# Kernel tuning notes

Hardware: AMD Instinct MI355X
Metric: run time of the kernel (lower is better)

Reference implementation:

```python
import jax, jax.numpy as jnp
import numpy as np

B, C, L = 4, 256, 4096
NUM_GROUPS = 32
EPS = 1e-6


def setup_inputs() -> dict:
    key = jax.random.key(0)
    ks = jax.random.split(key, 8)
    s = 1.0 / np.sqrt(C)  # conv1x1 init scale
    return {
        "x": jax.random.normal(ks[0], (B, C, L), dtype=jnp.float32),
        "norm_g": jnp.ones((C,), dtype=jnp.float32),
        "norm_b": jnp.zeros((C,), dtype=jnp.float32),
        "q_w": jax.random.normal(ks[1], (C, C), dtype=jnp.float32) * s,
        "q_b": jnp.zeros((C,), dtype=jnp.float32),
        "k_w": jax.random.normal(ks[2], (C, C), dtype=jnp.float32) * s,
        "k_b": jnp.zeros((C,), dtype=jnp.float32),
        "v_w": jax.random.normal(ks[3], (C, C), dtype=jnp.float32) * s,
        "v_b": jnp.zeros((C,), dtype=jnp.float32),
        "proj_w": jax.random.normal(ks[4], (C, C), dtype=jnp.float32) * s,
        "proj_b": jnp.zeros((C,), dtype=jnp.float32),
    }


def _group_norm(x, g, b):
    # x: [B, C, L] -> groups of C//NUM_GROUPS channels
    Bx, Cx, Lx = x.shape
    xg = x.reshape(Bx, NUM_GROUPS, Cx // NUM_GROUPS, Lx)
    mean = jnp.mean(xg, axis=(2, 3), keepdims=True)
    var = jnp.var(xg, axis=(2, 3), keepdims=True)
    xn = ((xg - mean) * jax.lax.rsqrt(var + EPS)).reshape(Bx, Cx, Lx)
    return xn * g[None, :, None] + b[None, :, None]


def _conv1x1(w, b, h):
    # w: [Cout, Cin], h: [B, Cin, L]
    return jnp.einsum("oc,bcl->bol", w, h) + b[None, :, None]


def reference(x, norm_g, norm_b, q_w, q_b, k_w, k_b, v_w, v_b, proj_w, proj_b):
    h = _group_norm(x, norm_g, norm_b)
    q = _conv1x1(q_w, q_b, h)   # [B, C, L]
    k = _conv1x1(k_w, k_b, h)
    v = _conv1x1(v_w, v_b, h)

    scale = jnp.asarray(x.shape[1], x.dtype) ** -0.5
    # w_[b,i,j] = sum_c q[b,c,i] * k[b,c,j]
    w_ = jnp.einsum("bci,bcj->bij", q, k) * scale
    w_ = jax.nn.softmax(w_, axis=2)
    # h_[b,c,i] = sum_j v[b,c,j] * w_[b,i,j]
    h2 = jnp.einsum("bcj,bij->bci", v, w_)

    out = _conv1x1(proj_w, proj_b, h2)
    return x + out
```

## Files before the change

kernel.cpp:

```cpp
#include <hip/hip_runtime.h>

#define B_ 4
#define C_ 256
#define L_ 4096
#define NG 32
#define CPG 8
#define BL (B_ * L_)
#define KPART 4
#define KEYS_PP (L_ / KPART)
#define QLOG2E 0.09016844f

typedef __attribute__((ext_vector_type(8))) __bf16 bf16x8;
typedef __attribute__((ext_vector_type(8))) short s16x8;
typedef __attribute__((ext_vector_type(4))) float f32x4;
typedef __attribute__((ext_vector_type(16))) float f32x16;

__device__ __forceinline__ unsigned short f2bf(float f) {
  unsigned int u = __builtin_bit_cast(unsigned int, f);
  u += 0x7fffu + ((u >> 16) & 1u);
  return (unsigned short)(u >> 16);
}
__device__ __forceinline__ float bf2f(unsigned short u) {
  unsigned int v = ((unsigned int)u) << 16;
  return __builtin_bit_cast(float, v);
}
#if __has_builtin(__builtin_amdgcn_exp2f)
#define EXP2F(x) __builtin_amdgcn_exp2f(x)
#else
#define EXP2F(x) exp2f(x)
#endif

__device__ __forceinline__ void gld_lds16(const void* g, void* l) {
  __builtin_amdgcn_global_load_lds(
      (const __attribute__((address_space(1))) unsigned int*)g,
      (__attribute__((address_space(3))) unsigned int*)l, 16, 0, 0);
}

__device__ __forceinline__ float red16_add(float x) {
  int i;
  i = __builtin_amdgcn_update_dpp(0, __builtin_bit_cast(int, x), 0xB1, 0xF, 0xF, false);
  x += __builtin_bit_cast(float, i);
  i = __builtin_amdgcn_update_dpp(0, __builtin_bit_cast(int, x), 0x4E, 0xF, 0xF, false);
  x += __builtin_bit_cast(float, i);
  i = __builtin_amdgcn_update_dpp(0, __builtin_bit_cast(int, x), 0x124, 0xF, 0xF, false);
  x += __builtin_bit_cast(float, i);
  i = __builtin_amdgcn_update_dpp(0, __builtin_bit_cast(int, x), 0x128, 0xF, 0xF, false);
  x += __builtin_bit_cast(float, i);
  return x;
}

__global__ __launch_bounds__(256) void init_k(const float* __restrict__ qw,
                                              const float* __restrict__ kw,
                                              const float* __restrict__ vw,
                                              const float* __restrict__ pw,
                                              const float* __restrict__ qb,
                                              const float* __restrict__ x,
                                              unsigned short* __restrict__ wq,
                                              unsigned short* __restrict__ wk,
                                              unsigned short* __restrict__ wv,
                                              unsigned short* __restrict__ wp,
                                              float* __restrict__ qbs,
                                              float* __restrict__ stats) {
  const int bid = blockIdx.x;
  const int t = threadIdx.x;
  if (bid < 128) {
    const int m = bid >> 5;
    const int blk = bid & 31;
    const float* src = (m == 0) ? qw : (m == 1) ? kw : (m == 2) ? vw : pw;
    unsigned short* dst = (m == 0) ? wq : (m == 1) ? wk : (m == 2) ? wv : wp;
    const float sc = (m == 0) ? QLOG2E : 1.0f;
    const int base = (blk * 256 + t) * 8;
    f32x4 a = *(const f32x4*)(src + base);
    f32x4 b = *(const f32x4*)(src + base + 4);
    s16x8 o;
#pragma unroll
    for (int j = 0; j < 4; ++j) {
      o[j] = (short)f2bf(a[j] * sc);
      o[4 + j] = (short)f2bf(b[j] * sc);
    }
    *(s16x8*)(dst + base) = o;
    if (m == 0 && blk == 0) qbs[t] = qb[t] * QLOG2E;
  } else {
    const int bg = bid - 128;
    const float* base = x + (size_t)bg * (CPG * L_);
    float s = 0.f, ss = 0.f;
#pragma unroll
    for (int i = 0; i < 32; ++i) {
      f32x4 v = *(const f32x4*)(base + (size_t)(t + i * 256) * 4);
#pragma unroll
      for (int j = 0; j < 4; ++j) { s += v[j]; ss += v[j] * v[j]; }
    }
#pragma unroll
    for (int d = 1; d < 64; d <<= 1) {
      s += __shfl_xor(s, d, 64);
      ss += __shfl_xor(ss, d, 64);
    }
    __shared__ float red[8];
    if ((t & 63) == 0) { red[(t >> 6) * 2] = s; red[(t >> 6) * 2 + 1] = ss; }
    __syncthreads();
    if (t == 0) {
      float S = red[0] + red[2] + red[4] + red[6];
      float SS = red[1] + red[3] + red[5] + red[7];
      const float inv_n = 1.f / (float)(CPG * L_);
      float mean = S * inv_n;
      float var = SS * inv_n - mean * mean;
      stats[bg * 2] = mean;
      stats[bg * 2 + 1] = rsqrtf(var + 1e-6f);
    }
  }
}

__global__ __launch_bounds__(256) void gn_apply_k(const float* __restrict__ x,
                                                  const float* __restrict__ stats,
                                                  const float* __restrict__ gam,
                                                  const float* __restrict__ bet,
                                                  unsigned short* __restrict__ ht) {
  __shared__ unsigned short tile[64 * 256];
  const int blk = blockIdx.x;
  const int b = blk >> 6;
  const int l0 = (blk & 63) * 64;
  const int t = threadIdx.x;
  const int c = t;
  const float mean = stats[(b * NG + (c >> 3)) * 2];
  const float rstd = stats[(b * NG + (c >> 3)) * 2 + 1];
  const float sc = rstd * gam[c];
  const float sb = bet[c] - mean * sc;
  const float* row = x + ((size_t)(b * C_ + c)) * L_ + l0;
#pragma unroll
  for (int v = 0; v < 16; ++v) {
    f32x4 f = *(const f32x4*)(row + v * 4);
#pragma unroll
    for (int j = 0; j < 4; ++j) tile[(v * 4 + j) * 256 + c] = f2bf(f[j] * sc + sb);
  }
  __syncthreads();
#pragma unroll
  for (int i = 0; i < 8; ++i) {
    int id = t + i * 256;
    int l = id >> 5, off = id & 31;
    *(s16x8*)(ht + ((size_t)(b * L_) + l0 + l) * 256 + off * 8) =
        *(const s16x8*)(tile + l * 256 + off * 8);
  }
}

__global__ __launch_bounds__(256) void qkv_k(const unsigned short* __restrict__ ht,
                                             const unsigned short* __restrict__ wq,
                                             const unsigned short* __restrict__ wk,
                                             const unsigned short* __restrict__ wv,
                                             const float* __restrict__ qbs,
                                             const float* __restrict__ kbias,
                                             const float* __restrict__ vbias,
                                             unsigned short* __restrict__ qt,
                                             unsigned short* __restrict__ kt,
                                             unsigned short* __restrict__ vg) {
  __shared__ unsigned short Al[64 * 256];
  __shared__ unsigned short Wl[64 * 256];
  const int z = blockIdx.z;
  const unsigned short* W = (z == 0) ? wq : (z == 1) ? wk : wv;
  const float* bias = (z == 0) ? qbs : (z == 1) ? kbias : vbias;
  const int m0 = blockIdx.x * 64;
  const int n0 = blockIdx.y * 64;
  const int t = threadIdx.x;
  const int w = t >> 6, lane = t & 63, l15 = lane & 15, q = lane >> 4;
#pragma unroll
  for (int i = 0; i < 8; ++i) {
    const int seg = w * 8 + i;
    const int idx = seg * 64 + lane;
    const int row = idx >> 5, c16 = idx & 31;
    gld_lds16(ht + (size_t)(m0 + row) * 256 + ((c16 ^ (row & 7)) * 8), Al + seg * 512);
    gld_lds16(W + (size_t)(n0 + row) * 256 + ((c16 ^ (row & 7)) * 8), Wl + seg * 512);
  }
  __syncthreads();
  bf16x8 af[8];
#pragma unroll
  for (int kf = 0; kf < 8; ++kf) {
    int row = w * 16 + l15;
    af[kf] = *(const bf16x8*)(Al + row * 256 + (((kf * 4 + q) ^ (row & 7)) * 8));
  }
  f32x4 acc[4];
#pragma unroll
  for (int nf = 0; nf < 4; ++nf) {
    f32x4 cacc = {0.f, 0.f, 0.f, 0.f};
#pragma unroll
    for (int kf = 0; kf < 8; ++kf) {
      int row = nf * 16 + l15;
      bf16x8 bf = *(const bf16x8*)(Wl + row * 256 + (((kf * 4 + q) ^ (row & 7)) * 8));
      cacc = __builtin_amdgcn_mfma_f32_16x16x32_bf16(af[kf], bf, cacc, 0, 0, 0);
    }
    acc[nf] = cacc;
  }
  unsigned short* Ct = (z == 0) ? qt : kt;
#pragma unroll
  for (int nf = 0; nf < 4; ++nf) {
    const int n = n0 + nf * 16 + l15;
    const float bs = bias[n];
#pragma unroll
    for (int r = 0; r < 4; ++r) {
      const int m = m0 + w * 16 + q * 4 + r;
      const float v = acc[nf][r] + bs;
      if (z < 2) {
        Ct[(size_t)m * 256 + n] = f2bf(v);
      } else {
        const int b = m >> 12, i = m & (L_ - 1);
        const int jt = i >> 5, jj = i & 31;
        const int qc = jj >> 3, pos = jj & 7;
        vg[((size_t)(b * 128 + jt)) * 8192 + n * 32 + ((qc ^ ((n >> 1) & 3)) * 8) + pos] =
            f2bf(v);
      }
    }
  }
}

__global__ __launch_bounds__(256) void proj_k(const unsigned short* __restrict__ X,
                                              const unsigned short* __restrict__ W,
                                              const float* __restrict__ bias,
                                              const float* __restrict__ xres,
                                              float* __restrict__ out) {
  __shared__ unsigned short Wl[64 * 256];
  __shared__ unsigned short Xl[64 * 256];
  const int i0 = blockIdx.x * 64;
  const int o0 = blockIdx.y * 64;
  const int b = blockIdx.z;
  const int t = threadIdx.x;
  const int w = t >> 6, lane = t & 63, l15 = lane & 15, q = lane >> 4;
#pragma unroll
  for (int i = 0; i < 8; ++i) {
    const int seg = w * 8 + i;
    const int idx = seg * 64 + lane;
    const int row = idx >> 5, c16 = idx & 31;
    gld_lds16(W + (size_t)(o0 + row) * 256 + ((c16 ^ (row & 7)) * 8), Wl + seg * 512);
    gld_lds16(X + ((size_t)(b * L_) + i0 + row) * 256 + ((c16 ^ (row & 7)) * 8),
              Xl + seg * 512);
  }
  __syncthreads();
  bf16x8 af[8];
#pragma unroll
  for (int kf = 0; kf < 8; ++kf) {
    int row = w * 16 + l15;
    af[kf] = *(const bf16x8*)(Wl + row * 256 + (((kf * 4 + q) ^ (row & 7)) * 8));
  }
  f32x4 acc[4];
#pragma unroll
  for (int nf = 0; nf < 4; ++nf) {
    f32x4 cacc = {0.f, 0.f, 0.f, 0.f};
#pragma unroll
    for (int kf = 0; kf < 8; ++kf) {
      int row = nf * 16 + l15;
      bf16x8 bf = *(const bf16x8*)(Xl + row * 256 + (((kf * 4 + q) ^ (row & 7)) * 8));
      cacc = __builtin_amdgcn_mfma_f32_16x16x32_bf16(af[kf], bf, cacc, 0, 0, 0);
    }
    acc[nf] = cacc;
  }
#pragma unroll
  for (int nf = 0; nf < 4; ++nf) {
    const int i = i0 + nf * 16 + l15;
#pragma unroll
    for (int r = 0; r < 4; ++r) {
      const int o = o0 + w * 16 + q * 4 + r;
      const size_t idx = ((size_t)(b * C_ + o)) * L_ + i;
      out[idx] = acc[nf][r] + bias[o] + xres[idx];
    }
  }
}

__global__ __launch_bounds__(256, 2) void attn_k(const unsigned short* __restrict__ Qt,
                                                 const unsigned short* __restrict__ Kt,
                                                 const unsigned short* __restrict__ Vg,
                                                 unsigned short* __restrict__ op01,
                                                 unsigned short* __restrict__ op23,
                                                 float* __restrict__ ml) {
  __shared__ unsigned short Kl[32 * 256];
  __shared__ unsigned short Vl[256 * 32];
  __shared__ unsigned short Pl[4 * 32 * 40];
  const int bid = blockIdx.x;
  const int g = bid & 15;
  const int b = g >> 2, part = g & 3;
  const int qi = bid >> 4;
  const int t = threadIdx.x;
  const int w = t >> 6, lane = t & 63;
  const int l15 = lane & 15, q = lane >> 4;
  const int l31 = lane & 31, h = lane >> 5;

  const int qrow0 = b * L_ + qi * 128 + w * 32;
  bf16x8 qf[2][8];
#pragma unroll
  for (int mi = 0; mi < 2; ++mi)
#pragma unroll
    for (int kf = 0; kf < 8; ++kf)
      qf[mi][kf] =
          *(const bf16x8*)(Qt + ((size_t)(qrow0 + mi * 16 + l15)) * 256 + kf * 32 + q * 8);

  f32x16 oacc[8];
#pragma unroll
  for (int nf = 0; nf < 8; ++nf)
#pragma unroll
    for (int gg = 0; gg < 16; ++gg) oacc[nf][gg] = 0.f;
  float ls0[4] = {0.f, 0.f, 0.f, 0.f}, ls1[4] = {0.f, 0.f, 0.f, 0.f};

  const unsigned short* kbase = Kt + ((size_t)(b * L_ + part * KEYS_PP)) * 256;
  const unsigned short* vbase = Vg + ((size_t)(b * 128 + part * 32)) * 8192;
  unsigned short* Pw = Pl + w * 1280;

  for (int it = 0; it < KEYS_PP / 32; ++it) {
    __syncthreads();
    {
      const unsigned short* ksrc = kbase + (size_t)(it * 32) * 256;
      const unsigned short* vsrc = vbase + (size_t)it * 8192;
#pragma unroll
      for (int i = 0; i < 4; ++i) {
        const int seg = w * 4 + i;
        const int idx = seg * 64 + lane;
        const int row = idx >> 5, c16 = idx & 31;
        gld_lds16(ksrc + (size_t)row * 256 + ((c16 ^ (row & 7)) * 8), Kl + seg * 512);
        gld_lds16(vsrc + (size_t)idx * 8, Vl + seg * 512);
      }
    }
    __syncthreads();

    f32x4 s00 = {0.f, 0.f, 0.f, 0.f}, s01 = s00, s10 = s00, s11 = s00;
#pragma unroll
    for (int kf = 0; kf < 8; ++kf) {
      const int ch = ((kf * 4 + q) ^ (l15 & 7)) * 8;
      bf16x8 kb0 = *(const bf16x8*)(Kl + l15 * 256 + ch);
      bf16x8 kb1 = *(const bf16x8*)(Kl + (16 + l15) * 256 + ch);
      s00 = __builtin_amdgcn_mfma_f32_16x16x32_bf16(qf[0][kf], kb0, s00, 0, 0, 0);
      s01 = __builtin_amdgcn_mfma_f32_16x16x32_bf16(qf[0][kf], kb1, s01, 0, 0, 0);
      s10 = __builtin_amdgcn_mfma_f32_16x16x32_bf16(qf[1][kf], kb0, s10, 0, 0, 0);
      s11 = __builtin_amdgcn_mfma_f32_16x16x32_bf16(qf[1][kf], kb1, s11, 0, 0, 0);
    }
#pragma unroll
    for (int r = 0; r < 4; ++r) {
      float p00 = EXP2F(s00[r]), p01 = EXP2F(s01[r]);
      float p10 = EXP2F(s10[r]), p11 = EXP2F(s11[r]);
      ls0[r] += p00 + p01;
      ls1[r] += p10 + p11;
      Pw[(q * 4 + r) * 40 + l15] = f2bf(p00);
      Pw[(q * 4 + r) * 40 + 16 + l15] = f2bf(p01);
      Pw[(16 + q * 4 + r) * 40 + l15] = f2bf(p10);
      Pw[(16 + q * 4 + r) * 40 + 16 + l15] = f2bf(p11);
    }
    __syncthreads();

    bf16x8 va[2][2];
#pragma unroll
    for (int nf = 0; nf < 2; ++nf) {
      const int c = w * 64 + nf * 32 + l31;
#pragma unroll
      for (int kc = 0; kc < 2; ++kc)
        va[nf][kc] =
            *(const bf16x8*)(Vl + c * 32 + (((kc * 2 + h) ^ ((c >> 1) & 3)) * 8));
    }
#pragma unroll
    for (int qt2 = 0; qt2 < 4; ++qt2) {
      bf16x8 pa0 = *(const bf16x8*)(Pl + qt2 * 1280 + l31 * 40 + h * 8);
      bf16x8 pa1 = *(const bf16x8*)(Pl + qt2 * 1280 + l31 * 40 + 16 + h * 8);
#pragma unroll
      for (int nf = 0; nf < 2; ++nf) {
        oacc[qt2 * 2 + nf] =
            __builtin_amdgcn_mfma_f32_32x32x16_bf16(pa0, va[nf][0], oacc[qt2 * 2 + nf], 0, 0, 0);
        oacc[qt2 * 2 + nf] =
            __builtin_amdgcn_mfma_f32_32x32x16_bf16(pa1, va[nf][1], oacc[qt2 * 2 + nf], 0, 0, 0);
      }
    }
  }

  unsigned short* opb = (part < 2) ? op01 + (size_t)part * BL * 256
                                   : op23 + (size_t)(part - 2) * BL * 256;
  const int qb0 = b * L_ + qi * 128;
#pragma unroll
  for (int qt2 = 0; qt2 < 4; ++qt2)
#pragma unroll
    for (int nf = 0; nf < 2; ++nf)
#pragma unroll
      for (int gg = 0; gg < 16; ++gg) {
        const int row = qt2 * 32 + (gg & 3) + 8 * (gg >> 2) + 4 * h;
        opb[(size_t)(qb0 + row) * 256 + w * 64 + nf * 32 + l31] =
            f2bf(oacc[qt2 * 2 + nf][gg]);
      }
#pragma unroll
  for (int r = 0; r < 4; ++r) {
    ls0[r] = red16_add(ls0[r]);
    ls1[r] = red16_add(ls1[r]);
  }
  if (l15 == 0) {
    float* mlp = ml + (size_t)part * BL;
#pragma unroll
    for (int r = 0; r < 4; ++r) {
      mlp[qrow0 + q * 4 + r] = ls0[r];
      mlp[qrow0 + 16 + q * 4 + r] = ls1[r];
    }
  }
}

__global__ __launch_bounds__(256) void merge_k(const unsigned short* __restrict__ op01,
                                               const unsigned short* __restrict__ op23,
                                               const float* __restrict__ ml,
                                               unsigned short* __restrict__ Om) {
  const int row = blockIdx.x * 8 + (threadIdx.x >> 5);
  const int c8 = threadIdx.x & 31;
  const float inv = 1.0f / (ml[row] + ml[BL + row] + ml[2 * BL + row] + ml[3 * BL + row]);
  const size_t off = (size_t)row * 256 + c8 * 8;
  s16x8 v0 = *(const s16x8*)(op01 + off);
  s16x8 v1 = *(const s16x8*)(op01 + (size_t)BL * 256 + off);
  s16x8 v2 = *(const s16x8*)(op23 + off);
  s16x8 v3 = *(const s16x8*)(op23 + (size_t)BL * 256 + off);
  s16x8 o;
#pragma unroll
  for (int j = 0; j < 8; ++j)
    o[j] = (short)f2bf((bf2f((unsigned short)v0[j]) + bf2f((unsigned short)v1[j]) +
                        bf2f((unsigned short)v2[j]) + bf2f((unsigned short)v3[j])) *
                       inv);
  *(s16x8*)(Om + off) = o;
}

extern "C" void kernel_launch(void* const* d_in, const int* in_sizes, int n_in,
                              void* d_out, int out_size, void* d_ws, size_t ws_size,
                              hipStream_t stream) {
  const float* x = (const float*)d_in[0];
  const float* norm_g = (const float*)d_in[1];
  const float* norm_b = (const float*)d_in[2];
  const float* q_w = (const float*)d_in[3];
  const float* q_b = (const float*)d_in[4];
  const float* k_w = (const float*)d_in[5];
  const float* k_b = (const float*)d_in[6];
  const float* v_w = (const float*)d_in[7];
  const float* v_b = (const float*)d_in[8];
  const float* p_w = (const float*)d_in[9];
  const float* p_b = (const float*)d_in[10];
  float* out = (float*)d_out;
  (void)in_sizes; (void)n_in; (void)out_size; (void)ws_size;

  char* ws = (char*)d_ws;
  const size_t MB = 1u << 20;
  float* stats = (float*)ws;
  float* qbs = (float*)(ws + 1024);
  unsigned short* wq = (unsigned short*)(ws + 4096);
  unsigned short* wk = wq + 65536;
  unsigned short* wv = wk + 65536;
  unsigned short* wp = wv + 65536;
  unsigned short* ht = (unsigned short*)(ws + 1 * MB);
  unsigned short* qt = (unsigned short*)(ws + 9 * MB);
  unsigned short* kt = (unsigned short*)(ws + 17 * MB);
  unsigned short* vg = (unsigned short*)(ws + 25 * MB);
  unsigned short* op23 = (unsigned short*)(ws + 33 * MB);
  float* ml = (float*)(ws + 50 * MB);
  unsigned short* op01 = (unsigned short*)d_out;

  init_k<<<256, 256, 0, stream>>>(q_w, k_w, v_w, p_w, q_b, x, wq, wk, wv, wp, qbs, stats);
  gn_apply_k<<<B_ * (L_ / 64), 256, 0, stream>>>(x, stats, norm_g, norm_b, ht);
  qkv_k<<<dim3((B_ * L_) / 64, C_ / 64, 3), 256, 0, stream>>>(ht, wq, wk, wv, qbs, k_b,
                                                              v_b, qt, kt, vg);
  attn_k<<<512, 256, 0, stream>>>(qt, kt, vg, op01, op23, ml);
  merge_k<<<BL / 8, 256, 0, stream>>>(op01, op23, ml, ht);
  proj_k<<<dim3(L_ / 64, C_ / 64, B_), 256, 0, stream>>>(ht, wp, p_b, x, out);
}
```

Before: 223.4 us.

## Fuse split-K merge into projection and pipeline V loads in attention

The attention kernel stops staging V through shared memory. Each wave reads V directly from global memory into registers in a new interleaved layout, and the P tile is double-buffered so the PV MFMAs for step it-1 run after the K prefetch for step it+1 is issued. When the workspace is large enough, the separate merge kernel is removed. The projection kernel instead accumulates over all four partial outputs and applies the softmax normaliser per row in its epilogue. This saves a kernel launch and one round trip of the merged tensor, but projection now does four times the MFMA work and LDS loads, and uncached V global reads may add latency.

```diff
diff --git a/kernel.cpp b/kernel.cpp
--- a/kernel.cpp
+++ b/kernel.cpp
@@ -8,6 +8,7 @@
 #define BL (B_ * L_)
 #define KPART 4
 #define KEYS_PP (L_ / KPART)
+#define NIT (KEYS_PP / 32)
 #define QLOG2E 0.09016844f
 
 typedef __attribute__((ext_vector_type(8))) __bf16 bf16x8;
@@ -201,19 +202,201 @@
         Ct[(size_t)m * 256 + n] = f2bf(v);
       } else {
         const int b = m >> 12, i = m & (L_ - 1);
-        const int jt = i >> 5, jj = i & 31;
-        const int qc = jj >> 3, pos = jj & 7;
-        vg[((size_t)(b * 128 + jt)) * 8192 + n * 32 + ((qc ^ ((n >> 1) & 3)) * 8) + pos] =
-            f2bf(v);
-      }
-    }
-  }
-}
-
+        const int jt = i >> 5, j = i & 31;
+        const int slot = (j & 15) * 2 + (j >> 4);
+        vg[((size_t)(b * 128 + jt)) * 8192 + n * 32 + slot] = f2bf(v);
+      }
+    }
+  }
+}
+
+__global__ __launch_bounds__(256, 2) void attn_k(const unsigned short* __restrict__ Qt,
+                                                 const unsigned short* __restrict__ Kt,
+                                                 const unsigned short* __restrict__ Vg,
+                                                 unsigned short* __restrict__ o0p,
+                                                 unsigned short* __restrict__ o1p,
+                                                 unsigned short* __restrict__ o2p,
+                                                 unsigned short* __restrict__ o3p,
+                                                 float* __restrict__ ml) {
+  __shared__ unsigned short Kl[32 * 256];
+  __shared__ unsigned int Pb[2][4][32][20];
+  const int bid = blockIdx.x;
+  const int g = bid & 15;
+  const int b = g >> 2, part = g & 3;
+  const int qi = bid >> 4;
+  const int t = threadIdx.x;
+  const int w = t >> 6, lane = t & 63;
+  const int l15 = lane & 15, q = lane >> 4;
+  const int l31 = lane & 31, h = lane >> 5;
+
+  const int qb0 = b * L_ + qi * 128;
+  const int qrow0 = qb0 + w * 32;
+  bf16x8 qf[2][8];
+#pragma unroll
+  for (int mi = 0; mi < 2; ++mi)
+#pragma unroll
+    for (int kf = 0; kf < 8; ++kf)
+      qf[mi][kf] =
+          *(const bf16x8*)(Qt + ((size_t)(qrow0 + mi * 16 + l15)) * 256 + kf * 32 + q * 8);
+
+  f32x16 oacc[8];
+#pragma unroll
+  for (int nf = 0; nf < 8; ++nf)
+#pragma unroll
+    for (int gg = 0; gg < 16; ++gg) oacc[nf][gg] = 0.f;
+  float ls0[4] = {0.f, 0.f, 0.f, 0.f}, ls1[4] = {0.f, 0.f, 0.f, 0.f};
+
+  const unsigned short* kbase = Kt + ((size_t)(b * L_ + part * KEYS_PP)) * 256;
+  const unsigned short* vbase = Vg + ((size_t)(b * 128 + part * 32)) * 8192;
+
+#pragma unroll
+  for (int i = 0; i < 4; ++i) {
+    const int seg = w * 4 + i;
+    const int idx = seg * 64 + lane;
+    const int row = idx >> 5, c16 = idx & 31;
+    gld_lds16(kbase + (size_t)row * 256 + ((c16 ^ (row & 7)) * 8), Kl + seg * 512);
+  }
+
+  for (int it = 0; it < NIT; ++it) {
+    __syncthreads();
+    bf16x8 va[2][2];
+    if (it > 0) {
+      const unsigned short* vt = vbase + (size_t)(it - 1) * 8192;
+#pragma unroll
+      for (int nf = 0; nf < 2; ++nf)
+#pragma unroll
+        for (int kc = 0; kc < 2; ++kc)
+          va[nf][kc] = *(const bf16x8*)(vt + (w * 64 + nf * 32 + l31) * 32 +
+                                        kc * 16 + h * 8);
+    }
+    f32x4 s00 = {0.f, 0.f, 0.f, 0.f}, s01 = s00, s10 = s00, s11 = s00;
+#pragma unroll
+    for (int kf = 0; kf < 8; ++kf) {
+      const int ch = ((kf * 4 + q) ^ (l15 & 7)) * 8;
+      bf16x8 kb0 = *(const bf16x8*)(Kl + l15 * 256 + ch);
+      bf16x8 kb1 = *(const bf16x8*)(Kl + (16 + l15) * 256 + ch);
+      s00 = __builtin_amdgcn_mfma_f32_16x16x32_bf16(qf[0][kf], kb0, s00, 0, 0, 0);
+      s01 = __builtin_amdgcn_mfma_f32_16x16x32_bf16(qf[0][kf], kb1, s01, 0, 0, 0);
+      s10 = __builtin_amdgcn_mfma_f32_16x16x32_bf16(qf[1][kf], kb0, s10, 0, 0, 0);
+      s11 = __builtin_amdgcn_mfma_f32_16x16x32_bf16(qf[1][kf], kb1, s11, 0, 0, 0);
+    }
+    const int buf = it & 1;
+#pragma unroll
+    for (int r = 0; r < 4; ++r) {
+      float p00 = EXP2F(s00[r]), p01 = EXP2F(s01[r]);
+      float p10 = EXP2F(s10[r]), p11 = EXP2F(s11[r]);
+      ls0[r] += p00 + p01;
+      ls1[r] += p10 + p11;
+      Pb[buf][w][q * 4 + r][l15] = (unsigned int)f2bf(p00) | ((unsigned int)f2bf(p01) << 16);
+      Pb[buf][w][16 + q * 4 + r][l15] =
+          (unsigned int)f2bf(p10) | ((unsigned int)f2bf(p11) << 16);
+    }
+    __syncthreads();
+    if (it + 1 < NIT) {
+      const unsigned short* ksrc = kbase + (size_t)((it + 1) * 32) * 256;
+#pragma unroll
+      for (int i = 0; i < 4; ++i) {
+        const int seg = w * 4 + i;
+        const int idx = seg * 64 + lane;
+        const int row = idx >> 5, c16 = idx & 31;
+        gld_lds16(ksrc + (size_t)row * 256 + ((c16 ^ (row & 7)) * 8), Kl + seg * 512);
+      }
+    }
+    if (it > 0) {
+      const int pbuf = (it - 1) & 1;
+#pragma unroll
+      for (int qt2 = 0; qt2 < 4; ++qt2) {
+        bf16x8 pa0 = *(const bf16x8*)&Pb[pbuf][qt2][l31][h * 4];
+        bf16x8 pa1 = *(const bf16x8*)&Pb[pbuf][qt2][l31][8 + h * 4];
+#pragma unroll
+        for (int nf = 0; nf < 2; ++nf) {
+          oacc[qt2 * 2 + nf] =
+              __builtin_amdgcn_mfma_f32_32x32x16_bf16(pa0, va[nf][0], oacc[qt2 * 2 + nf], 0, 0, 0);
+          oacc[qt2 * 2 + nf] =
+              __builtin_amdgcn_mfma_f32_32x32x16_bf16(pa1, va[nf][1], oacc[qt2 * 2 + nf], 0, 0, 0);
+        }
+      }
+    }
+  }
+  {
+    bf16x8 va[2][2];
+    const unsigned short* vt = vbase + (size_t)(NIT - 1) * 8192;
+#pragma unroll
+    for (int nf = 0; nf < 2; ++nf)
+#pragma unroll
+      for (int kc = 0; kc < 2; ++kc)
+        va[nf][kc] =
+            *(const bf16x8*)(vt + (w * 64 + nf * 32 + l31) * 32 + kc * 16 + h * 8);
+    const int pbuf = (NIT - 1) & 1;
+#pragma unroll
+    for (int qt2 = 0; qt2 < 4; ++qt2) {
+      bf16x8 pa0 = *(const bf16x8*)&Pb[pbuf][qt2][l31][h * 4];
+      bf16x8 pa1 = *(const bf16x8*)&Pb[pbuf][qt2][l31][8 + h * 4];
+#pragma unroll
+      for (int nf = 0; nf < 2; ++nf) {
+        oacc[qt2 * 2 + nf] =
+            __builtin_amdgcn_mfma_f32_32x32x16_bf16(pa0, va[nf][0], oacc[qt2 * 2 + nf], 0, 0, 0);
+        oacc[qt2 * 2 + nf] =
+            __builtin_amdgcn_mfma_f32_32x32x16_bf16(pa1, va[nf][1], oacc[qt2 * 2 + nf], 0, 0, 0);
+      }
+    }
+  }
+
+  unsigned short* opb = (part == 0) ? o0p : (part == 1) ? o1p : (part == 2) ? o2p : o3p;
+#pragma unroll
+  for (int qt2 = 0; qt2 < 4; ++qt2)
+#pragma unroll
+    for (int nf = 0; nf < 2; ++nf)
+#pragma unroll
+      for (int gg = 0; gg < 16; ++gg) {
+        const int row = qt2 * 32 + (gg & 3) + 8 * (gg >> 2) + 4 * h;
+        opb[(size_t)(qb0 + row) * 256 + w * 64 + nf * 32 + l31] =
+            f2bf(oacc[qt2 * 2 + nf][gg]);
+      }
+#pragma unroll
+  for (int r = 0; r < 4; ++r) {
+    ls0[r] = red16_add(ls0[r]);
+    ls1[r] = red16_add(ls1[r]);
+  }
+  if (l15 == 0) {
+    float* mlp = ml + (size_t)part * BL;
+#pragma unroll
+    for (int r = 0; r < 4; ++r) {
+      mlp[qrow0 + q * 4 + r] = ls0[r];
+      mlp[qrow0 + 16 + q * 4 + r] = ls1[r];
+    }
+  }
+}
+
+__global__ __launch_bounds__(256) void merge_k(const unsigned short* __restrict__ o0p,
+                                               const unsigned short* __restrict__ o1p,
+                                               const unsigned short* __restrict__ o2p,
+                                               const unsigned short* __restrict__ o3p,
+                                               const float* __restrict__ ml,
+                                               unsigned short* __restrict__ Om) {
+  const int row = blockIdx.x * 8 + (threadIdx.x >> 5);
+  const int c8 = threadIdx.x & 31;
+  const float inv = 1.0f / (ml[row] + ml[BL + row] + ml[2 * BL + row] + ml[3 * BL + row]);
+  const size_t off = (size_t)row * 256 + c8 * 8;
+  s16x8 v0 = *(const s16x8*)(o0p + off);
+  s16x8 v1 = *(const s16x8*)(o1p + off);
+  s16x8 v2 = *(const s16x8*)(o2p + off);
+  s16x8 v3 = *(const s16x8*)(o3p + off);
+  s16x8 o;
+#pragma unroll
+  for (int j = 0; j < 8; ++j)
+    o[j] = (short)f2bf((bf2f((unsigned short)v0[j]) + bf2f((unsigned short)v1[j]) +
+                        bf2f((unsigned short)v2[j]) + bf2f((unsigned short)v3[j])) *
+                       inv);
+  *(s16x8*)(Om + off) = o;
+}
+
+template <int FUSED>
 __global__ __launch_bounds__(256) void proj_k(const unsigned short* __restrict__ X,
                                               const unsigned short* __restrict__ W,
                                               const float* __restrict__ bias,
                                               const float* __restrict__ xres,
+                                              const float* __restrict__ ml,
                                               float* __restrict__ out) {
   __shared__ unsigned short Wl[64 * 256];
   __shared__ unsigned short Xl[64 * 256];
@@ -222,6 +405,7 @@
   const int b = blockIdx.z;
   const int t = threadIdx.x;
   const int w = t >> 6, lane = t & 63, l15 = lane & 15, q = lane >> 4;
+  const int NP = FUSED ? 4 : 1;
 #pragma unroll
   for (int i = 0; i < 8; ++i) {
     const int seg = w * 8 + i;
@@ -238,178 +422,48 @@
     int row = w * 16 + l15;
     af[kf] = *(const bf16x8*)(Wl + row * 256 + (((kf * 4 + q) ^ (row & 7)) * 8));
   }
-  f32x4 acc[4];
-#pragma unroll
-  for (int nf = 0; nf < 4; ++nf) {
-    f32x4 cacc = {0.f, 0.f, 0.f, 0.f};
-#pragma unroll
-    for (int kf = 0; kf < 8; ++kf) {
-      int row = nf * 16 + l15;
-      bf16x8 bf = *(const bf16x8*)(Xl + row * 256 + (((kf * 4 + q) ^ (row & 7)) * 8));
-      cacc = __builtin_amdgcn_mfma_f32_16x16x32_bf16(af[kf], bf, cacc, 0, 0, 0);
-    }
-    acc[nf] = cacc;
+  f32x4 acc[4] = {{0.f, 0.f, 0.f, 0.f}, {0.f, 0.f, 0.f, 0.f},
+                  {0.f, 0.f, 0.f, 0.f}, {0.f, 0.f, 0.f, 0.f}};
+  for (int p = 0; p < NP; ++p) {
+    if (p > 0) {
+      __syncthreads();
+#pragma unroll
+      for (int i = 0; i < 8; ++i) {
+        const int seg = w * 8 + i;
+        const int idx = seg * 64 + lane;
+        const int row = idx >> 5, c16 = idx & 31;
+        gld_lds16(X + ((size_t)p * BL + (size_t)(b * L_) + i0 + row) * 256 +
+                      ((c16 ^ (row & 7)) * 8),
+                  Xl + seg * 512);
+      }
+      __syncthreads();
+    }
+#pragma unroll
+    for (int nf = 0; nf < 4; ++nf) {
+      f32x4 cacc = acc[nf];
+#pragma unroll
+      for (int kf = 0; kf < 8; ++kf) {
+        int row = nf * 16 + l15;
+        bf16x8 bf = *(const bf16x8*)(Xl + row * 256 + (((kf * 4 + q) ^ (row & 7)) * 8));
+        cacc = __builtin_amdgcn_mfma_f32_16x16x32_bf16(af[kf], bf, cacc, 0, 0, 0);
+      }
+      acc[nf] = cacc;
+    }
   }
 #pragma unroll
   for (int nf = 0; nf < 4; ++nf) {
     const int i = i0 + nf * 16 + l15;
+    const int grow = b * L_ + i;
+    float sc = 1.0f;
+    if (FUSED)
+      sc = 1.0f / (ml[grow] + ml[BL + grow] + ml[2 * BL + grow] + ml[3 * BL + grow]);
 #pragma unroll
     for (int r = 0; r < 4; ++r) {
       const int o = o0 + w * 16 + q * 4 + r;
       const size_t idx = ((size_t)(b * C_ + o)) * L_ + i;
-      out[idx] = acc[nf][r] + bias[o] + xres[idx];
-    }
-  }
-}
-
-__global__ __launch_bounds__(256, 2) void attn_k(const unsigned short* __restrict__ Qt,
-                                                 const unsigned short* __restrict__ Kt,
-                                                 const unsigned short* __restrict__ Vg,
-                                                 unsigned short* __restrict__ op01,
-                                                 unsigned short* __restrict__ op23,
-                                                 float* __restrict__ ml) {
-  __shared__ unsigned short Kl[32 * 256];
-  __shared__ unsigned short Vl[256 * 32];
-  __shared__ unsigned short Pl[4 * 32 * 40];
-  const int bid = blockIdx.x;
-  const int g = bid & 15;
-  const int b = g >> 2, part = g & 3;
-  const int qi = bid >> 4;
-  const int t = threadIdx.x;
-  const int w = t >> 6, lane = t & 63;
-  const int l15 = lane & 15, q = lane >> 4;
-  const int l31 = lane & 31, h = lane >> 5;
-
-  const int qrow0 = b * L_ + qi * 128 + w * 32;
-  bf16x8 qf[2][8];
-#pragma unroll
-  for (int mi = 0; mi < 2; ++mi)
-#pragma unroll
-    for (int kf = 0; kf < 8; ++kf)
-      qf[mi][kf] =
-          *(const bf16x8*)(Qt + ((size_t)(qrow0 + mi * 16 + l15)) * 256 + kf * 32 + q * 8);
-
-  f32x16 oacc[8];
-#pragma unroll
-  for (int nf = 0; nf < 8; ++nf)
-#pragma unroll
-    for (int gg = 0; gg < 16; ++gg) oacc[nf][gg] = 0.f;
-  float ls0[4] = {0.f, 0.f, 0.f, 0.f}, ls1[4] = {0.f, 0.f, 0.f, 0.f};
-
-  const unsigned short* kbase = Kt + ((size_t)(b * L_ + part * KEYS_PP)) * 256;
-  const unsigned short* vbase = Vg + ((size_t)(b * 128 + part * 32)) * 8192;
-  unsigned short* Pw = Pl + w * 1280;
-
-  for (int it = 0; it < KEYS_PP / 32; ++it) {
-    __syncthreads();
-    {
-      const unsigned short* ksrc = kbase + (size_t)(it * 32) * 256;
-      const unsigned short* vsrc = vbase + (size_t)it * 8192;
-#pragma unroll
-      for (int i = 0; i < 4; ++i) {
-        const int seg = w * 4 + i;
-        const int idx = seg * 64 + lane;
-        const int row = idx >> 5, c16 = idx & 31;
-        gld_lds16(ksrc + (size_t)row * 256 + ((c16 ^ (row & 7)) * 8), Kl + seg * 512);
-        gld_lds16(vsrc + (size_t)idx * 8, Vl + seg * 512);
-      }
-    }
-    __syncthreads();
-
-    f32x4 s00 = {0.f, 0.f, 0.f, 0.f}, s01 = s00, s10 = s00, s11 = s00;
-#pragma unroll
-    for (int kf = 0; kf < 8; ++kf) {
-      const int ch = ((kf * 4 + q) ^ (l15 & 7)) * 8;
-      bf16x8 kb0 = *(const bf16x8*)(Kl + l15 * 256 + ch);
-      bf16x8 kb1 = *(const bf16x8*)(Kl + (16 + l15) * 256 + ch);
-      s00 = __builtin_amdgcn_mfma_f32_16x16x32_bf16(qf[0][kf], kb0, s00, 0, 0, 0);
-      s01 = __builtin_amdgcn_mfma_f32_16x16x32_bf16(qf[0][kf], kb1, s01, 0, 0, 0);
-      s10 = __builtin_amdgcn_mfma_f32_16x16x32_bf16(qf[1][kf], kb0, s10, 0, 0, 0);
-      s11 = __builtin_amdgcn_mfma_f32_16x16x32_bf16(qf[1][kf], kb1, s11, 0, 0, 0);
-    }
-#pragma unroll
-    for (int r = 0; r < 4; ++r) {
-      float p00 = EXP2F(s00[r]), p01 = EXP2F(s01[r]);
-      float p10 = EXP2F(s10[r]), p11 = EXP2F(s11[r]);
-      ls0[r] += p00 + p01;
-      ls1[r] += p10 + p11;
-      Pw[(q * 4 + r) * 40 + l15] = f2bf(p00);
-      Pw[(q * 4 + r) * 40 + 16 + l15] = f2bf(p01);
-      Pw[(16 + q * 4 + r) * 40 + l15] = f2bf(p10);
-      Pw[(16 + q * 4 + r) * 40 + 16 + l15] = f2bf(p11);
-    }
-    __syncthreads();
-
-    bf16x8 va[2][2];
-#pragma unroll
-    for (int nf = 0; nf < 2; ++nf) {
-      const int c = w * 64 + nf * 32 + l31;
-#pragma unroll
-      for (int kc = 0; kc < 2; ++kc)
-        va[nf][kc] =
-            *(const bf16x8*)(Vl + c * 32 + (((kc * 2 + h) ^ ((c >> 1) & 3)) * 8));
-    }
-#pragma unroll
-    for (int qt2 = 0; qt2 < 4; ++qt2) {
-      bf16x8 pa0 = *(const bf16x8*)(Pl + qt2 * 1280 + l31 * 40 + h * 8);
-      bf16x8 pa1 = *(const bf16x8*)(Pl + qt2 * 1280 + l31 * 40 + 16 + h * 8);
-#pragma unroll
-      for (int nf = 0; nf < 2; ++nf) {
-        oacc[qt2 * 2 + nf] =
-            __builtin_amdgcn_mfma_f32_32x32x16_bf16(pa0, va[nf][0], oacc[qt2 * 2 + nf], 0, 0, 0);
-        oacc[qt2 * 2 + nf] =
-            __builtin_amdgcn_mfma_f32_32x32x16_bf16(pa1, va[nf][1], oacc[qt2 * 2 + nf], 0, 0, 0);
-      }
-    }
-  }
-
-  unsigned short* opb = (part < 2) ? op01 + (size_t)part * BL * 256
-                                   : op23 + (size_t)(part - 2) * BL * 256;
-  const int qb0 = b * L_ + qi * 128;
-#pragma unroll
-  for (int qt2 = 0; qt2 < 4; ++qt2)
-#pragma unroll
-    for (int nf = 0; nf < 2; ++nf)
-#pragma unroll
-      for (int gg = 0; gg < 16; ++gg) {
-        const int row = qt2 * 32 + (gg & 3) + 8 * (gg >> 2) + 4 * h;
-        opb[(size_t)(qb0 + row) * 256 + w * 64 + nf * 32 + l31] =
-            f2bf(oacc[qt2 * 2 + nf][gg]);
-      }
-#pragma unroll
-  for (int r = 0; r < 4; ++r) {
-    ls0[r] = red16_add(ls0[r]);
-    ls1[r] = red16_add(ls1[r]);
-  }
-  if (l15 == 0) {
-    float* mlp = ml + (size_t)part * BL;
-#pragma unroll
-    for (int r = 0; r < 4; ++r) {
-      mlp[qrow0 + q * 4 + r] = ls0[r];
-      mlp[qrow0 + 16 + q * 4 + r] = ls1[r];
-    }
-  }
-}
-
-__global__ __launch_bounds__(256) void merge_k(const unsigned short* __restrict__ op01,
-                                               const unsigned short* __restrict__ op23,
-                                               const float* __restrict__ ml,
-                                               unsigned short* __restrict__ Om) {
-  const int row = blockIdx.x * 8 + (threadIdx.x >> 5);
-  const int c8 = threadIdx.x & 31;
-  const float inv = 1.0f / (ml[row] + ml[BL + row] + ml[2 * BL + row] + ml[3 * BL + row]);
-  const size_t off = (size_t)row * 256 + c8 * 8;
-  s16x8 v0 = *(const s16x8*)(op01 + off);
-  s16x8 v1 = *(const s16x8*)(op01 + (size_t)BL * 256 + off);
-  s16x8 v2 = *(const s16x8*)(op23 + off);
-  s16x8 v3 = *(const s16x8*)(op23 + (size_t)BL * 256 + off);
-  s16x8 o;
-#pragma unroll
-  for (int j = 0; j < 8; ++j)
-    o[j] = (short)f2bf((bf2f((unsigned short)v0[j]) + bf2f((unsigned short)v1[j]) +
-                        bf2f((unsigned short)v2[j]) + bf2f((unsigned short)v3[j])) *
-                       inv);
-  *(s16x8*)(Om + off) = o;
+      out[idx] = acc[nf][r] * sc + bias[o] + xres[idx];
+    }
+  }
 }
 
 extern "C" void kernel_launch(void* const* d_in, const int* in_sizes, int n_in,
@@ -427,29 +481,48 @@
   const float* p_w = (const float*)d_in[9];
   const float* p_b = (const float*)d_in[10];
   float* out = (float*)d_out;
-  (void)in_sizes; (void)n_in; (void)out_size; (void)ws_size;
+  (void)in_sizes; (void)n_in; (void)out_size;
 
   char* ws = (char*)d_ws;
   const size_t MB = 1u << 20;
+  const size_t PSZ = (size_t)BL * 256 * 2;
   float* stats = (float*)ws;
   float* qbs = (float*)(ws + 1024);
   unsigned short* wq = (unsigned short*)(ws + 4096);
   unsigned short* wk = wq + 65536;
   unsigned short* wv = wk + 65536;
   unsigned short* wp = wv + 65536;
+  float* ml = (float*)(ws + 640 * 1024);
   unsigned short* ht = (unsigned short*)(ws + 1 * MB);
   unsigned short* qt = (unsigned short*)(ws + 9 * MB);
   unsigned short* kt = (unsigned short*)(ws + 17 * MB);
   unsigned short* vg = (unsigned short*)(ws + 25 * MB);
-  unsigned short* op23 = (unsigned short*)(ws + 33 * MB);
-  float* ml = (float*)(ws + 50 * MB);
-  unsigned short* op01 = (unsigned short*)d_out;
+
+  const int fused = (ws_size >= 33 * MB + 4 * PSZ) ? 1 : 0;
+
+  unsigned short *o0p, *o1p, *o2p, *o3p;
+  if (fused) {
+    unsigned short* opcat = (unsigned short*)(ws + 33 * MB);
+    o0p = opcat;
+    o1p = opcat + PSZ / 2;
+    o2p = opcat + PSZ;
+    o3p = opcat + 3 * PSZ / 2;
+  } else {
+    o0p = (unsigned short*)d_out;
+    o1p = (unsigned short*)d_out + PSZ / 2;
+    o2p = (unsigned short*)(ws + 33 * MB);
+    o3p = o2p + PSZ / 2;
+  }
 
   init_k<<<256, 256, 0, stream>>>(q_w, k_w, v_w, p_w, q_b, x, wq, wk, wv, wp, qbs, stats);
   gn_apply_k<<<B_ * (L_ / 64), 256, 0, stream>>>(x, stats, norm_g, norm_b, ht);
   qkv_k<<<dim3((B_ * L_) / 64, C_ / 64, 3), 256, 0, stream>>>(ht, wq, wk, wv, qbs, k_b,
                                                               v_b, qt, kt, vg);
-  attn_k<<<512, 256, 0, stream>>>(qt, kt, vg, op01, op23, ml);
-  merge_k<<<BL / 8, 256, 0, stream>>>(op01, op23, ml, ht);
-  proj_k<<<dim3(L_ / 64, C_ / 64, B_), 256, 0, stream>>>(ht, wp, p_b, x, out);
-}
+  attn_k<<<512, 256, 0, stream>>>(qt, kt, vg, o0p, o1p, o2p, o3p, ml);
+  if (fused) {
+    proj_k<1><<<dim3(L_ / 64, C_ / 64, B_), 256, 0, stream>>>(o0p, wp, p_b, x, ml, out);
+  } else {
+    merge_k<<<BL / 8, 256, 0, stream>>>(o0p, o1p, o2p, o3p, ml, ht);
+    proj_k<0><<<dim3(L_ / 64, C_ / 64, B_), 256, 0, stream>>>(ht, wp, p_b, x, ml, out);
+  }
+}
```

New measurement: 237.9 us. 1.07x slower.

## Double-buffer K/V tiles and make each wave own its query rows in PV

Applied to the files above, without the earlier changes.

The attention kernel now double-buffers the K and V shared-memory tiles, prefetching the next key block while the current one is computed. This removes one of the two barriers per iteration. The PV step is restructured so each wave multiplies only its own 32 query rows against all 256 channels, which removes the barrier before reading other waves' P tiles. The cost is twice the LDS for K/V, which may lower occupancy below the requested 2 blocks/CU, and more V reads from LDS per wave. The partial-output buffer pointers and the ml location are also reorganized.

```diff
diff --git a/kernel.cpp b/kernel.cpp
--- a/kernel.cpp
+++ b/kernel.cpp
@@ -8,6 +8,7 @@
 #define BL (B_ * L_)
 #define KPART 4
 #define KEYS_PP (L_ / KPART)
+#define NIT (KEYS_PP / 32)
 #define QLOG2E 0.09016844f
 
 typedef __attribute__((ext_vector_type(8))) __bf16 bf16x8;
@@ -210,6 +211,155 @@
   }
 }
 
+__global__ __launch_bounds__(256, 2) void attn_k(const unsigned short* __restrict__ Qt,
+                                                 const unsigned short* __restrict__ Kt,
+                                                 const unsigned short* __restrict__ Vg,
+                                                 unsigned short* __restrict__ o0p,
+                                                 unsigned short* __restrict__ o1p,
+                                                 unsigned short* __restrict__ o2p,
+                                                 unsigned short* __restrict__ o3p,
+                                                 float* __restrict__ ml) {
+  __shared__ unsigned short Kl[2][32 * 256];
+  __shared__ unsigned short Vl[2][256 * 32];
+  __shared__ unsigned short Pl[4 * 32 * 40];
+  const int bid = blockIdx.x;
+  const int g = bid & 15;
+  const int b = g >> 2, part = g & 3;
+  const int qi = bid >> 4;
+  const int t = threadIdx.x;
+  const int w = t >> 6, lane = t & 63;
+  const int l15 = lane & 15, q = lane >> 4;
+  const int l31 = lane & 31, h = lane >> 5;
+
+  const int qb0 = b * L_ + qi * 128;
+  const int qrow0 = qb0 + w * 32;
+  bf16x8 qf[2][8];
+#pragma unroll
+  for (int mi = 0; mi < 2; ++mi)
+#pragma unroll
+    for (int kf = 0; kf < 8; ++kf)
+      qf[mi][kf] =
+          *(const bf16x8*)(Qt + ((size_t)(qrow0 + mi * 16 + l15)) * 256 + kf * 32 + q * 8);
+
+  f32x16 oacc[8];
+#pragma unroll
+  for (int nf = 0; nf < 8; ++nf)
+#pragma unroll
+    for (int gg = 0; gg < 16; ++gg) oacc[nf][gg] = 0.f;
+  float ls0[4] = {0.f, 0.f, 0.f, 0.f}, ls1[4] = {0.f, 0.f, 0.f, 0.f};
+
+  const unsigned short* kbase = Kt + ((size_t)(b * L_ + part * KEYS_PP)) * 256;
+  const unsigned short* vbase = Vg + ((size_t)(b * 128 + part * 32)) * 8192;
+  unsigned short* Pw = Pl + w * 1280;
+
+#pragma unroll
+  for (int i = 0; i < 4; ++i) {
+    const int seg = w * 4 + i;
+    const int idx = seg * 64 + lane;
+    const int row = idx >> 5, c16 = idx & 31;
+    gld_lds16(kbase + (size_t)row * 256 + ((c16 ^ (row & 7)) * 8), &Kl[0][0] + seg * 512);
+    gld_lds16(vbase + (size_t)idx * 8, &Vl[0][0] + seg * 512);
+  }
+
+  for (int it = 0; it < NIT; ++it) {
+    __syncthreads();
+    if (it + 1 < NIT) {
+      const unsigned short* ksrc = kbase + (size_t)((it + 1) * 32) * 256;
+      const unsigned short* vsrc = vbase + (size_t)(it + 1) * 8192;
+      unsigned short* kd = &Kl[(it + 1) & 1][0];
+      unsigned short* vd = &Vl[(it + 1) & 1][0];
+#pragma unroll
+      for (int i = 0; i < 4; ++i) {
+        const int seg = w * 4 + i;
+        const int idx = seg * 64 + lane;
+        const int row = idx >> 5, c16 = idx & 31;
+        gld_lds16(ksrc + (size_t)row * 256 + ((c16 ^ (row & 7)) * 8), kd + seg * 512);
+        gld_lds16(vsrc + (size_t)idx * 8, vd + seg * 512);
+      }
+    }
+    const unsigned short* Kb = &Kl[it & 1][0];
+    const unsigned short* Vb = &Vl[it & 1][0];
+
+    f32x4 s00 = {0.f, 0.f, 0.f, 0.f}, s01 = s00, s10 = s00, s11 = s00;
+#pragma unroll
+    for (int kf = 0; kf < 8; ++kf) {
+      const int ch = ((kf * 4 + q) ^ (l15 & 7)) * 8;
+      bf16x8 kb0 = *(const bf16x8*)(Kb + l15 * 256 + ch);
+      bf16x8 kb1 = *(const bf16x8*)(Kb + (16 + l15) * 256 + ch);
+      s00 = __builtin_amdgcn_mfma_f32_16x16x32_bf16(qf[0][kf], kb0, s00, 0, 0, 0);
+      s01 = __builtin_amdgcn_mfma_f32_16x16x32_bf16(qf[0][kf], kb1, s01, 0, 0, 0);
+      s10 = __builtin_amdgcn_mfma_f32_16x16x32_bf16(qf[1][kf], kb0, s10, 0, 0, 0);
+      s11 = __builtin_amdgcn_mfma_f32_16x16x32_bf16(qf[1][kf], kb1, s11, 0, 0, 0);
+    }
+#pragma unroll
+    for (int r = 0; r < 4; ++r) {
+      float p00 = EXP2F(s00[r]), p01 = EXP2F(s01[r]);
+      float p10 = EXP2F(s10[r]), p11 = EXP2F(s11[r]);
+      ls0[r] += p00 + p01;
+      ls1[r] += p10 + p11;
+      Pw[(q * 4 + r) * 40 + l15] = f2bf(p00);
+      Pw[(q * 4 + r) * 40 + 16 + l15] = f2bf(p01);
+      Pw[(16 + q * 4 + r) * 40 + l15] = f2bf(p10);
+      Pw[(16 + q * 4 + r) * 40 + 16 + l15] = f2bf(p11);
+    }
+    bf16x8 pa0 = *(const bf16x8*)(Pw + l31 * 40 + h * 8);
+    bf16x8 pa1 = *(const bf16x8*)(Pw + l31 * 40 + 16 + h * 8);
+#pragma unroll
+    for (int nf = 0; nf < 8; ++nf) {
+      const int c = nf * 32 + l31;
+      bf16x8 v0 = *(const bf16x8*)(Vb + c * 32 + ((h ^ ((c >> 1) & 3)) * 8));
+      bf16x8 v1 = *(const bf16x8*)(Vb + c * 32 + (((2 + h) ^ ((c >> 1) & 3)) * 8));
+      oacc[nf] = __builtin_amdgcn_mfma_f32_32x32x16_bf16(pa0, v0, oacc[nf], 0, 0, 0);
+      oacc[nf] = __builtin_amdgcn_mfma_f32_32x32x16_bf16(pa1, v1, oacc[nf], 0, 0, 0);
+    }
+  }
+
+  unsigned short* opb = (part == 0) ? o0p : (part == 1) ? o1p : (part == 2) ? o2p : o3p;
+#pragma unroll
+  for (int nf = 0; nf < 8; ++nf)
+#pragma unroll
+    for (int gg = 0; gg < 16; ++gg) {
+      const int row = (gg & 3) + 8 * (gg >> 2) + 4 * h;
+      opb[(size_t)(qrow0 + row) * 256 + nf * 32 + l31] = f2bf(oacc[nf][gg]);
+    }
+#pragma unroll
+  for (int r = 0; r < 4; ++r) {
+    ls0[r] = red16_add(ls0[r]);
+    ls1[r] = red16_add(ls1[r]);
+  }
+  if (l15 == 0) {
+    float* mlp = ml + (size_t)part * BL;
+#pragma unroll
+    for (int r = 0; r < 4; ++r) {
+      mlp[qrow0 + q * 4 + r] = ls0[r];
+      mlp[qrow0 + 16 + q * 4 + r] = ls1[r];
+    }
+  }
+}
+
+__global__ __launch_bounds__(256) void merge_k(const unsigned short* __restrict__ o0p,
+                                               const unsigned short* __restrict__ o1p,
+                                               const unsigned short* __restrict__ o2p,
+                                               const unsigned short* __restrict__ o3p,
+                                               const float* __restrict__ ml,
+                                               unsigned short* __restrict__ Om) {
+  const int row = blockIdx.x * 8 + (threadIdx.x >> 5);
+  const int c8 = threadIdx.x & 31;
+  const float inv = 1.0f / (ml[row] + ml[BL + row] + ml[2 * BL + row] + ml[3 * BL + row]);
+  const size_t off = (size_t)row * 256 + c8 * 8;
+  s16x8 v0 = *(const s16x8*)(o0p + off);
+  s16x8 v1 = *(const s16x8*)(o1p + off);
+  s16x8 v2 = *(const s16x8*)(o2p + off);
+  s16x8 v3 = *(const s16x8*)(o3p + off);
+  s16x8 o;
+#pragma unroll
+  for (int j = 0; j < 8; ++j)
+    o[j] = (short)f2bf((bf2f((unsigned short)v0[j]) + bf2f((unsigned short)v1[j]) +
+                        bf2f((unsigned short)v2[j]) + bf2f((unsigned short)v3[j])) *
+                       inv);
+  *(s16x8*)(Om + off) = o;
+}
+
 __global__ __launch_bounds__(256) void proj_k(const unsigned short* __restrict__ X,
                                               const unsigned short* __restrict__ W,
                                               const float* __restrict__ bias,
@@ -260,156 +410,6 @@
       out[idx] = acc[nf][r] + bias[o] + xres[idx];
     }
   }
-}
-
-__global__ __launch_bounds__(256, 2) void attn_k(const unsigned short* __restrict__ Qt,
-                                                 const unsigned short* __restrict__ Kt,
-                                                 const unsigned short* __restrict__ Vg,
-                                                 unsigned short* __restrict__ op01,
-                                                 unsigned short* __restrict__ op23,
-                                                 float* __restrict__ ml) {
-  __shared__ unsigned short Kl[32 * 256];
-  __shared__ unsigned short Vl[256 * 32];
-  __shared__ unsigned short Pl[4 * 32 * 40];
-  const int bid = blockIdx.x;
-  const int g = bid & 15;
-  const int b = g >> 2, part = g & 3;
-  const int qi = bid >> 4;
-  const int t = threadIdx.x;
-  const int w = t >> 6, lane = t & 63;
-  const int l15 = lane & 15, q = lane >> 4;
-  const int l31 = lane & 31, h = lane >> 5;
-
-  const int qrow0 = b * L_ + qi * 128 + w * 32;
-  bf16x8 qf[2][8];
-#pragma unroll
-  for (int mi = 0; mi < 2; ++mi)
-#pragma unroll
-    for (int kf = 0; kf < 8; ++kf)
-      qf[mi][kf] =
-          *(const bf16x8*)(Qt + ((size_t)(qrow0 + mi * 16 + l15)) * 256 + kf * 32 + q * 8);
-
-  f32x16 oacc[8];
-#pragma unroll
-  for (int nf = 0; nf < 8; ++nf)
-#pragma unroll
-    for (int gg = 0; gg < 16; ++gg) oacc[nf][gg] = 0.f;
-  float ls0[4] = {0.f, 0.f, 0.f, 0.f}, ls1[4] = {0.f, 0.f, 0.f, 0.f};
-
-  const unsigned short* kbase = Kt + ((size_t)(b * L_ + part * KEYS_PP)) * 256;
-  const unsigned short* vbase = Vg + ((size_t)(b * 128 + part * 32)) * 8192;
-  unsigned short* Pw = Pl + w * 1280;
-
-  for (int it = 0; it < KEYS_PP / 32; ++it) {
-    __syncthreads();
-    {
-      const unsigned short* ksrc = kbase + (size_t)(it * 32) * 256;
-      const unsigned short* vsrc = vbase + (size_t)it * 8192;
-#pragma unroll
-      for (int i = 0; i < 4; ++i) {
-        const int seg = w * 4 + i;
-        const int idx = seg * 64 + lane;
-        const int row = idx >> 5, c16 = idx & 31;
-        gld_lds16(ksrc + (size_t)row * 256 + ((c16 ^ (row & 7)) * 8), Kl + seg * 512);
-        gld_lds16(vsrc + (size_t)idx * 8, Vl + seg * 512);
-      }
-    }
-    __syncthreads();
-
-    f32x4 s00 = {0.f, 0.f, 0.f, 0.f}, s01 = s00, s10 = s00, s11 = s00;
-#pragma unroll
-    for (int kf = 0; kf < 8; ++kf) {
-      const int ch = ((kf * 4 + q) ^ (l15 & 7)) * 8;
-      bf16x8 kb0 = *(const bf16x8*)(Kl + l15 * 256 + ch);
-      bf16x8 kb1 = *(const bf16x8*)(Kl + (16 + l15) * 256 + ch);
-      s00 = __builtin_amdgcn_mfma_f32_16x16x32_bf16(qf[0][kf], kb0, s00, 0, 0, 0);
-      s01 = __builtin_amdgcn_mfma_f32_16x16x32_bf16(qf[0][kf], kb1, s01, 0, 0, 0);
-      s10 = __builtin_amdgcn_mfma_f32_16x16x32_bf16(qf[1][kf], kb0, s10, 0, 0, 0);
-      s11 = __builtin_amdgcn_mfma_f32_16x16x32_bf16(qf[1][kf], kb1, s11, 0, 0, 0);
-    }
-#pragma unroll
-    for (int r = 0; r < 4; ++r) {
-      float p00 = EXP2F(s00[r]), p01 = EXP2F(s01[r]);
-      float p10 = EXP2F(s10[r]), p11 = EXP2F(s11[r]);
-      ls0[r] += p00 + p01;
-      ls1[r] += p10 + p11;
-      Pw[(q * 4 + r) * 40 + l15] = f2bf(p00);
-      Pw[(q * 4 + r) * 40 + 16 + l15] = f2bf(p01);
-      Pw[(16 + q * 4 + r) * 40 + l15] = f2bf(p10);
-      Pw[(16 + q * 4 + r) * 40 + 16 + l15] = f2bf(p11);
-    }
-    __syncthreads();
-
-    bf16x8 va[2][2];
-#pragma unroll
-    for (int nf = 0; nf < 2; ++nf) {
-      const int c = w * 64 + nf * 32 + l31;
-#pragma unroll
-      for (int kc = 0; kc < 2; ++kc)
-        va[nf][kc] =
-            *(const bf16x8*)(Vl + c * 32 + (((kc * 2 + h) ^ ((c >> 1) & 3)) * 8));
-    }
-#pragma unroll
-    for (int qt2 = 0; qt2 < 4; ++qt2) {
-      bf16x8 pa0 = *(const bf16x8*)(Pl + qt2 * 1280 + l31 * 40 + h * 8);
-      bf16x8 pa1 = *(const bf16x8*)(Pl + qt2 * 1280 + l31 * 40 + 16 + h * 8);
-#pragma unroll
-      for (int nf = 0; nf < 2; ++nf) {
-        oacc[qt2 * 2 + nf] =
-            __builtin_amdgcn_mfma_f32_32x32x16_bf16(pa0, va[nf][0], oacc[qt2 * 2 + nf], 0, 0, 0);
-        oacc[qt2 * 2 + nf] =
-            __builtin_amdgcn_mfma_f32_32x32x16_bf16(pa1, va[nf][1], oacc[qt2 * 2 + nf], 0, 0, 0);
-      }
-    }
-  }
-
-  unsigned short* opb = (part < 2) ? op01 + (size_t)part * BL * 256
-                                   : op23 + (size_t)(part - 2) * BL * 256;
-  const int qb0 = b * L_ + qi * 128;
-#pragma unroll
-  for (int qt2 = 0; qt2 < 4; ++qt2)
-#pragma unroll
-    for (int nf = 0; nf < 2; ++nf)
-#pragma unroll
-      for (int gg = 0; gg < 16; ++gg) {
-        const int row = qt2 * 32 + (gg & 3) + 8 * (gg >> 2) + 4 * h;
-        opb[(size_t)(qb0 + row) * 256 + w * 64 + nf * 32 + l31] =
-            f2bf(oacc[qt2 * 2 + nf][gg]);
-      }
-#pragma unroll
-  for (int r = 0; r < 4; ++r) {
-    ls0[r] = red16_add(ls0[r]);
-    ls1[r] = red16_add(ls1[r]);
-  }
-  if (l15 == 0) {
-    float* mlp = ml + (size_t)part * BL;
-#pragma unroll
-    for (int r = 0; r < 4; ++r) {
-      mlp[qrow0 + q * 4 + r] = ls0[r];
-      mlp[qrow0 + 16 + q * 4 + r] = ls1[r];
-    }
-  }
-}
-
-__global__ __launch_bounds__(256) void merge_k(const unsigned short* __restrict__ op01,
-                                               const unsigned short* __restrict__ op23,
-                                               const float* __restrict__ ml,
-                                               unsigned short* __restrict__ Om) {
-  const int row = blockIdx.x * 8 + (threadIdx.x >> 5);
-  const int c8 = threadIdx.x & 31;
-  const float inv = 1.0f / (ml[row] + ml[BL + row] + ml[2 * BL + row] + ml[3 * BL + row]);
-  const size_t off = (size_t)row * 256 + c8 * 8;
-  s16x8 v0 = *(const s16x8*)(op01 + off);
-  s16x8 v1 = *(const s16x8*)(op01 + (size_t)BL * 256 + off);
-  s16x8 v2 = *(const s16x8*)(op23 + off);
-  s16x8 v3 = *(const s16x8*)(op23 + (size_t)BL * 256 + off);
-  s16x8 o;
-#pragma unroll
-  for (int j = 0; j < 8; ++j)
-    o[j] = (short)f2bf((bf2f((unsigned short)v0[j]) + bf2f((unsigned short)v1[j]) +
-                        bf2f((unsigned short)v2[j]) + bf2f((unsigned short)v3[j])) *
-                       inv);
-  *(s16x8*)(Om + off) = o;
 }
 
 extern "C" void kernel_launch(void* const* d_in, const int* in_sizes, int n_in,
@@ -431,25 +431,28 @@
 
   char* ws = (char*)d_ws;
   const size_t MB = 1u << 20;
+  const size_t PSZ = (size_t)BL * 256 * 2;
   float* stats = (float*)ws;
   float* qbs = (float*)(ws + 1024);
   unsigned short* wq = (unsigned short*)(ws + 4096);
   unsigned short* wk = wq + 65536;
   unsigned short* wv = wk + 65536;
   unsigned short* wp = wv + 65536;
+  float* ml = (float*)(ws + 640 * 1024);
   unsigned short* ht = (unsigned short*)(ws + 1 * MB);
   unsigned short* qt = (unsigned short*)(ws + 9 * MB);
   unsigned short* kt = (unsigned short*)(ws + 17 * MB);
   unsigned short* vg = (unsigned short*)(ws + 25 * MB);
-  unsigned short* op23 = (unsigned short*)(ws + 33 * MB);
-  float* ml = (float*)(ws + 50 * MB);
-  unsigned short* op01 = (unsigned short*)d_out;
+  unsigned short* o0p = (unsigned short*)d_out;
+  unsigned short* o1p = o0p + PSZ / 2;
+  unsigned short* o2p = (unsigned short*)(ws + 33 * MB);
+  unsigned short* o3p = o2p + PSZ / 2;
 
   init_k<<<256, 256, 0, stream>>>(q_w, k_w, v_w, p_w, q_b, x, wq, wk, wv, wp, qbs, stats);
   gn_apply_k<<<B_ * (L_ / 64), 256, 0, stream>>>(x, stats, norm_g, norm_b, ht);
   qkv_k<<<dim3((B_ * L_) / 64, C_ / 64, 3), 256, 0, stream>>>(ht, wq, wk, wv, qbs, k_b,
                                                               v_b, qt, kt, vg);
-  attn_k<<<512, 256, 0, stream>>>(qt, kt, vg, op01, op23, ml);
-  merge_k<<<BL / 8, 256, 0, stream>>>(op01, op23, ml, ht);
+  attn_k<<<512, 256, 0, stream>>>(qt, kt, vg, o0p, o1p, o2p, o3p, ml);
+  merge_k<<<BL / 8, 256, 0, stream>>>(o0p, o1p, o2p, o3p, ml, ht);
   proj_k<<<dim3(L_ / 64, C_ / 64, B_), 256, 0, stream>>>(ht, wp, p_b, x, out);
 }
```

Result: no change. 220.9 us (-1.1%).
